# Performance work log

Measured on AMD Instinct MI355X. Metric: run time of the kernel, lower is better.

Reference implementation:

```python
import jax, jax.numpy as jnp
import numpy as np

B, S, IN_DIM, OUT_DIM = 4, 8192, 1024, 1024


def setup_inputs() -> dict:
    key = jax.random.key(0)
    kx, km, kv, kt = jax.random.split(key, 4)
    x = jax.random.normal(kx, (B, S, IN_DIM), dtype=jnp.float32)
    visual_mask = jax.random.randint(km, (B, S), 0, 2) > 0  # bool [B, S]
    # nn.Linear(in_dim, out_dim, bias=False): weight shape [out_dim, in_dim]
    bound = 1.0 / np.sqrt(IN_DIM)
    W_v = jax.random.uniform(kv, (OUT_DIM, IN_DIM), dtype=jnp.float32, minval=-bound, maxval=bound)
    W_t = jax.random.uniform(kt, (OUT_DIM, IN_DIM), dtype=jnp.float32, minval=-bound, maxval=bound)
    return {"x": x, "visual_mask": visual_mask, "W_v": W_v, "W_t": W_t}


def reference(x, visual_mask, W_v, W_t):
    # out = linear_v(x) * mask + linear_t(x) * ~mask
    y_v = jnp.einsum("bsd,od->bso", x, W_v)  # [B, S, OUT_DIM]
    y_t = jnp.einsum("bsd,od->bso", x, W_t)
    m = visual_mask[:, :, None]  # [B, S, 1]
    return jnp.where(m, y_v, y_t)
```

## Files before the change

kernel.cpp:

```cpp
#include <hip/hip_runtime.h>
#include <hip/hip_bf16.h>
#include <stdint.h>

#define M_TOT  32768
#define K_DIM  1024
#define N_DIM  1024

typedef short bf16x8 __attribute__((ext_vector_type(8)));
typedef float f32x4  __attribute__((ext_vector_type(4)));

#define AS1(p) ((__attribute__((address_space(1))) void*)(p))
#define AS3(p) ((__attribute__((address_space(3))) void*)(p))

__device__ __forceinline__ uint32_t packbf2(float a, float b) {
    __hip_bfloat162 h = __float22bfloat162_rn(make_float2(a, b));
    union { __hip_bfloat162 h; uint32_t u; } cvt;
    cvt.h = h;
    return cvt.u;
}

__global__ __launch_bounds__(1024) void prep_kernel(
        const int* __restrict__ mask,
        const float* __restrict__ wv, const float* __restrict__ wt,
        ushort* __restrict__ dv, ushort* __restrict__ dt,
        int* __restrict__ V, int* __restrict__ T, int* __restrict__ cnt) {
    const int b   = blockIdx.x;
    const int tid = threadIdx.x;

    if (b < 32) {
        const int lane = tid & 63;
        const int wv_i = tid >> 6;

        int pre = 0;
        const int nPre4 = b * 256;
        for (int i = tid; i < nPre4; i += 1024) {
            int4 v = ((const int4*)mask)[i];
            pre += (v.x != 0) + (v.y != 0) + (v.z != 0) + (v.w != 0);
        }
#pragma unroll
        for (int d = 32; d > 0; d >>= 1) pre += __shfl_down(pre, d);
        __shared__ int wsum[16];
        __shared__ int pref_s;
        if (lane == 0) wsum[wv_i] = pre;
        __syncthreads();
        if (tid == 0) {
            int s = 0;
#pragma unroll
            for (int i = 0; i < 16; ++i) s += wsum[i];
            pref_s = s;
        }
        __syncthreads();
        const int prefix_v = pref_s;

        const int e   = b * 1024 + tid;
        const int bit = (mask[e] != 0) ? 1 : 0;
        unsigned long long bal = __ballot(bit);
        const int lexcl = __popcll(bal & ((1ull << lane) - 1ull));
        const int wcnt  = __popcll(bal);
        __shared__ int wc[16];
        if (lane == 0) wc[wv_i] = wcnt;
        __syncthreads();
        int wpre = 0;
        for (int i = 0; i < wv_i; ++i) wpre += wc[i];
        int chunk_tot = 0;
#pragma unroll
        for (int i = 0; i < 16; ++i) chunk_tot += wc[i];
        const int gv = prefix_v + wpre + lexcl;
        if (bit) V[gv]     = e;
        else     T[e - gv] = e;

        if (b == 31) {
            const int Nv = prefix_v + chunk_tot;
            const int Nt = M_TOT - Nv;
            if (tid == 0) { cnt[0] = Nv; cnt[1] = Nt; }
            const int NBv = (Nv + 127) >> 7, NBt = (Nt + 127) >> 7;
            for (int p = Nv + tid; p < NBv * 128; p += 1024) V[p] = -1;
            for (int p = Nt + tid; p < NBt * 128; p += 1024) T[p] = -1;
        }
        return;
    }

    int u = (b - 32) * 8192 + tid * 8;
    const float* src; ushort* dst; int off;
    if (u < 1048576) { src = wv; dst = dv; off = u; }
    else             { src = wt; dst = dt; off = u - 1048576; }
    float4 a0 = *(const float4*)(src + off);
    float4 a1 = *(const float4*)(src + off + 4);
    uint4 p;
    p.x = packbf2(a0.x, a0.y);
    p.y = packbf2(a0.z, a0.w);
    p.z = packbf2(a1.x, a1.y);
    p.w = packbf2(a1.z, a1.w);
    *(uint4*)(dst + off) = p;
}

__global__ __launch_bounds__(256) void gemm_kernel(
        const float*  __restrict__ x,
        const ushort* __restrict__ Wv,
        const ushort* __restrict__ Wt,
        const int*    __restrict__ V,
        const int*    __restrict__ T,
        const int*    __restrict__ cnt,
        float*        __restrict__ out) {
    __shared__ float  sA[128 * 64];
    __shared__ ushort sB[128 * 64];

    const int tid  = threadIdx.x;
    const int lane = tid & 63;
    const int w    = tid >> 6;

    const int kx = blockIdx.x & 7;
    const int bn = (blockIdx.x >> 3) & 7;
    const int gk = blockIdx.x >> 6;
    const int bm = gk * 8 + kx;

    const int Nv  = cnt[0];
    const int Nt  = cnt[1];
    const int NBv = (Nv + 127) >> 7;
    const int NBt = (Nt + 127) >> 7;
    if (bm >= NBv + NBt) return;

    const bool vis = (bm < NBv);
    const int*    rowbase = vis ? (V + (size_t)bm * 128)
                                : (T + (size_t)(bm - NBv) * 128);
    const ushort* W       = vis ? Wv : Wt;
    const int n0 = bn * 128;

    const int arow = tid >> 4;
    const int akc  = (tid & 15) ^ arow;
    const float* ap8[8];
#pragma unroll
    for (int r = 0; r < 8; ++r) {
        int rr = rowbase[r * 16 + arow];
        if (rr < 0) rr = 0;
        ap8[r] = x + (size_t)rr * K_DIM + akc * 4;
    }
    const int trow = tid >> 3;
    const int kcb  = (tid & 7) ^ (trow & 7);
    const ushort* wp[4];
#pragma unroll
    for (int r = 0; r < 4; ++r) {
        wp[r] = W + (size_t)(n0 + r * 32 + trow) * K_DIM + kcb * 8;
    }

    const int ml   = lane & 15;
    const int quad = lane >> 4;
    const int wm = (w & 1) * 64;
    const int wn = (w >> 1) * 64;
    uint32_t aoff[2][4], boff[2][4];
#pragma unroll
    for (int ks = 0; ks < 2; ++ks) {
        const int kc0 = ks * 8 + quad * 2;
        const int kxr = (ks * 4 + quad) ^ (ml & 7);
#pragma unroll
        for (int t = 0; t < 4; ++t) {
            aoff[ks][t] = (uint32_t)(((wm + t * 16 + ml) * 16 + (kc0 ^ ml)) * 16);
            boff[ks][t] = (uint32_t)(((wn + t * 16 + ml) * 8 + kxr) * 16);
        }
    }

    f32x4 acc[4][4];
#pragma unroll
    for (int i = 0; i < 4; ++i)
#pragma unroll
        for (int j = 0; j < 4; ++j) {
            f32x4 z = {0.f, 0.f, 0.f, 0.f};
            acc[i][j] = z;
        }

    char* sAb = (char*)sA;
    char* sBb = (char*)sB;

    for (int kt = 0; kt < 16; ++kt) {
        const int k0 = kt * 64;
#pragma unroll
        for (int r = 0; r < 4; ++r) {
            char* lb = sBb + (size_t)(r * 256 + w * 64) * 16;
            __builtin_amdgcn_global_load_lds(AS1(wp[r] + k0), AS3(lb), 16, 0, 0);
        }
#pragma unroll
        for (int r = 0; r < 8; ++r) {
            char* la = sAb + (size_t)(r * 256 + w * 64) * 16;
            __builtin_amdgcn_global_load_lds(AS1(ap8[r] + k0), AS3(la), 16, 0, 0);
        }
        __syncthreads();
#pragma unroll
        for (int ks = 0; ks < 2; ++ks) {
            bf16x8 af[4], bf[4];
#pragma unroll
            for (int t = 0; t < 4; ++t) {
                f32x4 lo = *(const f32x4*)(sAb + aoff[ks][t]);
                f32x4 hi = *(const f32x4*)(sAb + (aoff[ks][t] ^ 16u));
                union { uint32_t u[4]; bf16x8 v; } cv;
                cv.u[0] = packbf2(lo[0], lo[1]);
                cv.u[1] = packbf2(lo[2], lo[3]);
                cv.u[2] = packbf2(hi[0], hi[1]);
                cv.u[3] = packbf2(hi[2], hi[3]);
                af[t] = cv.v;
            }
#pragma unroll
            for (int t = 0; t < 4; ++t) bf[t] = *(const bf16x8*)(sBb + boff[ks][t]);
#pragma unroll
            for (int tm = 0; tm < 4; ++tm)
#pragma unroll
                for (int tn = 0; tn < 4; ++tn)
                    acc[tm][tn] = __builtin_amdgcn_mfma_f32_16x16x32_bf16(
                        af[tm], bf[tn], acc[tm][tn], 0, 0, 0);
        }
        __syncthreads();
    }

#pragma unroll
    for (int tm = 0; tm < 4; ++tm) {
        const int rb = wm + tm * 16 + quad * 4;
        int sr0 = rowbase[rb + 0];
        int sr1 = rowbase[rb + 1];
        int sr2 = rowbase[rb + 2];
        int sr3 = rowbase[rb + 3];
#pragma unroll
        for (int tn = 0; tn < 4; ++tn) {
            const int col = n0 + wn + tn * 16 + ml;
            if (sr0 >= 0) out[(size_t)sr0 * N_DIM + col] = acc[tm][tn][0];
            if (sr1 >= 0) out[(size_t)sr1 * N_DIM + col] = acc[tm][tn][1];
            if (sr2 >= 0) out[(size_t)sr2 * N_DIM + col] = acc[tm][tn][2];
            if (sr3 >= 0) out[(size_t)sr3 * N_DIM + col] = acc[tm][tn][3];
        }
    }
}

extern "C" void kernel_launch(void* const* d_in, const int* in_sizes, int n_in,
                              void* d_out, int out_size, void* d_ws, size_t ws_size,
                              hipStream_t stream) {
    const float* x    = (const float*)d_in[0];
    const int*   mask = (const int*)d_in[1];
    const float* Wv   = (const float*)d_in[2];
    const float* Wt   = (const float*)d_in[3];
    float* out = (float*)d_out;

    char* ws = (char*)d_ws;
    ushort* dWv = (ushort*)(ws);
    ushort* dWt = (ushort*)(ws + (1 << 21));
    int* V   = (int*)(ws + (1 << 22));
    int* T   = V + 32768;
    int* cnt = T + 32768;

    prep_kernel<<<288, 1024, 0, stream>>>(mask, Wv, Wt, dWv, dWt, V, T, cnt);
    gemm_kernel<<<33 * 64, 256, 0, stream>>>(x, dWv, dWt, V, T, cnt, out);
}
```

Before: 380.4 us.

## Double-buffer LDS tiles with K=32 stages to overlap loads and MFMA

Splits the K=64 LDS tile into two K=32 buffers and issues the global-to-LDS loads for the next stage before computing on the current one, so memory latency overlaps with MFMA work. Swizzle patterns and load thread mappings are reworked for the narrower tiles. The total LDS footprint stays the same. The cost is twice as many barriers per K sweep and shorter compute phases between them.

```diff
diff --git a/kernel.cpp b/kernel.cpp
--- a/kernel.cpp
+++ b/kernel.cpp
@@ -102,8 +102,8 @@
         const int*    __restrict__ T,
         const int*    __restrict__ cnt,
         float*        __restrict__ out) {
-    __shared__ float  sA[128 * 64];
-    __shared__ ushort sB[128 * 64];
+    __shared__ float  sA[2][128 * 32];
+    __shared__ ushort sB[2][128 * 32];
 
     const int tid  = threadIdx.x;
     const int lane = tid & 63;
@@ -126,37 +126,34 @@
     const ushort* W       = vis ? Wv : Wt;
     const int n0 = bn * 128;
 
-    const int arow = tid >> 4;
-    const int akc  = (tid & 15) ^ arow;
-    const float* ap8[8];
-#pragma unroll
-    for (int r = 0; r < 8; ++r) {
-        int rr = rowbase[r * 16 + arow];
+    const int arow = tid >> 3;
+    const int akc  = (tid & 7) ^ (arow & 7);
+    const float* ap[4];
+#pragma unroll
+    for (int r = 0; r < 4; ++r) {
+        int rr = rowbase[r * 32 + arow];
         if (rr < 0) rr = 0;
-        ap8[r] = x + (size_t)rr * K_DIM + akc * 4;
-    }
-    const int trow = tid >> 3;
-    const int kcb  = (tid & 7) ^ (trow & 7);
-    const ushort* wp[4];
-#pragma unroll
-    for (int r = 0; r < 4; ++r) {
-        wp[r] = W + (size_t)(n0 + r * 32 + trow) * K_DIM + kcb * 8;
+        ap[r] = x + (size_t)rr * K_DIM + akc * 4;
+    }
+    const int brow = tid >> 2;
+    const int bkc  = (tid & 3) ^ (brow & 3);
+    const ushort* wp[2];
+#pragma unroll
+    for (int r = 0; r < 2; ++r) {
+        wp[r] = W + (size_t)(n0 + r * 64 + brow) * K_DIM + bkc * 8;
     }
 
     const int ml   = lane & 15;
     const int quad = lane >> 4;
     const int wm = (w & 1) * 64;
     const int wn = (w >> 1) * 64;
-    uint32_t aoff[2][4], boff[2][4];
-#pragma unroll
-    for (int ks = 0; ks < 2; ++ks) {
-        const int kc0 = ks * 8 + quad * 2;
-        const int kxr = (ks * 4 + quad) ^ (ml & 7);
-#pragma unroll
-        for (int t = 0; t < 4; ++t) {
-            aoff[ks][t] = (uint32_t)(((wm + t * 16 + ml) * 16 + (kc0 ^ ml)) * 16);
-            boff[ks][t] = (uint32_t)(((wn + t * 16 + ml) * 8 + kxr) * 16);
-        }
+    uint32_t aoff[4], boff[4];
+#pragma unroll
+    for (int t = 0; t < 4; ++t) {
+        const int am = wm + t * 16 + ml;
+        const int an = wn + t * 16 + ml;
+        aoff[t] = (uint32_t)((am * 8 + ((2 * quad) ^ (am & 7))) * 16);
+        boff[t] = (uint32_t)((an * 4 + (quad ^ (an & 3))) * 16);
     }
 
     f32x4 acc[4][4];
@@ -168,47 +165,63 @@
             acc[i][j] = z;
         }
 
-    char* sAb = (char*)sA;
-    char* sBb = (char*)sB;
-
-    for (int kt = 0; kt < 16; ++kt) {
-        const int k0 = kt * 64;
-#pragma unroll
-        for (int r = 0; r < 4; ++r) {
-            char* lb = sBb + (size_t)(r * 256 + w * 64) * 16;
-            __builtin_amdgcn_global_load_lds(AS1(wp[r] + k0), AS3(lb), 16, 0, 0);
-        }
-#pragma unroll
-        for (int r = 0; r < 8; ++r) {
-            char* la = sAb + (size_t)(r * 256 + w * 64) * 16;
-            __builtin_amdgcn_global_load_lds(AS1(ap8[r] + k0), AS3(la), 16, 0, 0);
-        }
-        __syncthreads();
-#pragma unroll
-        for (int ks = 0; ks < 2; ++ks) {
-            bf16x8 af[4], bf[4];
-#pragma unroll
-            for (int t = 0; t < 4; ++t) {
-                f32x4 lo = *(const f32x4*)(sAb + aoff[ks][t]);
-                f32x4 hi = *(const f32x4*)(sAb + (aoff[ks][t] ^ 16u));
-                union { uint32_t u[4]; bf16x8 v; } cv;
-                cv.u[0] = packbf2(lo[0], lo[1]);
-                cv.u[1] = packbf2(lo[2], lo[3]);
-                cv.u[2] = packbf2(hi[0], hi[1]);
-                cv.u[3] = packbf2(hi[2], hi[3]);
-                af[t] = cv.v;
-            }
-#pragma unroll
-            for (int t = 0; t < 4; ++t) bf[t] = *(const bf16x8*)(sBb + boff[ks][t]);
-#pragma unroll
-            for (int tm = 0; tm < 4; ++tm)
-#pragma unroll
-                for (int tn = 0; tn < 4; ++tn)
-                    acc[tm][tn] = __builtin_amdgcn_mfma_f32_16x16x32_bf16(
-                        af[tm], bf[tn], acc[tm][tn], 0, 0, 0);
-        }
-        __syncthreads();
-    }
+    char* sA0 = (char*)sA[0];
+    char* sA1 = (char*)sA[1];
+    char* sB0 = (char*)sB[0];
+    char* sB1 = (char*)sB[1];
+
+#define STAGE(SAB, SBB, T)                                                      \
+    {                                                                           \
+        const int kA = (T) * 32;                                                \
+        _Pragma("unroll")                                                       \
+        for (int r = 0; r < 4; ++r) {                                           \
+            char* la = (SAB) + (size_t)(r * 256 + tid) * 16;                    \
+            __builtin_amdgcn_global_load_lds(AS1(ap[r] + kA), AS3(la), 16, 0, 0);\
+        }                                                                       \
+        _Pragma("unroll")                                                       \
+        for (int r = 0; r < 2; ++r) {                                           \
+            char* lb = (SBB) + (size_t)(r * 256 + tid) * 16;                    \
+            __builtin_amdgcn_global_load_lds(AS1(wp[r] + kA), AS3(lb), 16, 0, 0);\
+        }                                                                       \
+    }
+
+#define COMPUTE(SAB, SBB)                                                       \
+    {                                                                           \
+        bf16x8 af[4], bf[4];                                                    \
+        _Pragma("unroll")                                                       \
+        for (int t = 0; t < 4; ++t) {                                           \
+            f32x4 lo = *(const f32x4*)((SAB) + aoff[t]);                        \
+            f32x4 hi = *(const f32x4*)((SAB) + (aoff[t] ^ 16u));                \
+            union { uint32_t u[4]; bf16x8 v; } cv;                              \
+            cv.u[0] = packbf2(lo[0], lo[1]);                                    \
+            cv.u[1] = packbf2(lo[2], lo[3]);                                    \
+            cv.u[2] = packbf2(hi[0], hi[1]);                                    \
+            cv.u[3] = packbf2(hi[2], hi[3]);                                    \
+            af[t] = cv.v;                                                       \
+        }                                                                       \
+        _Pragma("unroll")                                                       \
+        for (int t = 0; t < 4; ++t) bf[t] = *(const bf16x8*)((SBB) + boff[t]);  \
+        _Pragma("unroll")                                                       \
+        for (int tm = 0; tm < 4; ++tm)                                          \
+            _Pragma("unroll")                                                   \
+            for (int tn = 0; tn < 4; ++tn)                                      \
+                acc[tm][tn] = __builtin_amdgcn_mfma_f32_16x16x32_bf16(          \
+                    af[tm], bf[tn], acc[tm][tn], 0, 0, 0);                      \
+    }
+
+    STAGE(sA0, sB0, 0);
+    __syncthreads();
+
+    for (int tt = 0; tt < 32; tt += 2) {
+        STAGE(sA1, sB1, tt + 1);
+        COMPUTE(sA0, sB0);
+        __syncthreads();
+        if (tt + 2 < 32) STAGE(sA0, sB0, tt + 2);
+        COMPUTE(sA1, sB1);
+        __syncthreads();
+    }
+#undef STAGE
+#undef COMPUTE
 
 #pragma unroll
     for (int tm = 0; tm < 4; ++tm) {
```

Measured after the change: 413.0 us. 8.6% more time.
